# Kernel optimization log

Measured on AMD Instinct MI355X. Metric: run time of the kernel, lower is better.

The kernel has to match this reference:

```python
import jax, jax.numpy as jnp
import numpy as np
import math

IN_FEATURES = 4096
OUT_FEATURES = 4096
TOKENS = 8192


def hadamard(x):
    """Orthonormal fast Walsh-Hadamard transform along last dim (power of two)."""
    n = x.shape[-1]
    orig_shape = x.shape
    y = x.reshape(-1, n)
    h = 1
    while h < n:  # log2(n) butterfly steps (static loop, n known at trace time)
        y = y.reshape(-1, n // (2 * h), 2 * h)
        left = y[..., :h]
        right = y[..., h:2 * h]
        y = jnp.concatenate([left + right, left - right], axis=-1)
        y = y.reshape(-1, n)
        h *= 2
    return (y / math.sqrt(n)).reshape(orig_shape)


def setup_inputs() -> dict:
    key = jax.random.key(0)
    k1, k2, k3, k4 = jax.random.split(key, 4)
    x = jax.random.normal(k1, (TOKENS, IN_FEATURES), dtype=jnp.float32)
    # int8-valued quantized weights, stored as int32 for portability
    Q_tilde = jax.random.randint(k2, (OUT_FEATURES, IN_FEATURES), -127, 128, dtype=jnp.int32)
    # per-row scales, positive, realistic magnitude (~max_abs/127)
    s_tilde = jax.random.uniform(k3, (OUT_FEATURES, 1), dtype=jnp.float32, minval=0.001, maxval=0.02)
    bias = jax.random.normal(k4, (OUT_FEATURES,), dtype=jnp.float32)
    return {"x": x, "Q_tilde": Q_tilde, "s_tilde": s_tilde, "bias": bias}


def reference(x, Q_tilde, s_tilde, bias):
    # y = hadamard(x) @ (Q * s)^T + bias
    xh = hadamard(x)                                      # [T, in]
    W = Q_tilde.astype(jnp.float32) * s_tilde             # [out, in] dequantized
    y = xh @ W.T + bias                                   # [T, out]
    return y
```

## Files before the change

kernel.cpp:

```cpp
#include <hip/hip_runtime.h>
#include <hip/hip_bf16.h>

typedef int   i32x4 __attribute__((ext_vector_type(4)));
typedef unsigned int   u32;
typedef unsigned short u16;
typedef signed char    i8;

#define TOKENS 8192
#define NDIM   4096
#define KDIM   4096
#define BK     64
#define NKT    (KDIM / BK)

__device__ __forceinline__ u32 pack4(int4 q) {
  return (u32)(q.x & 0xff) | ((u32)(q.y & 0xff) << 8) |
         ((u32)(q.z & 0xff) << 16) | ((u32)(q.w & 0xff) << 24);
}

__global__ __launch_bounds__(256)
void fused_aux(const float* __restrict__ x, i8* __restrict__ xq,
               float* __restrict__ xscale,
               const int* __restrict__ Q, i8* __restrict__ W8) {
  __shared__ float tbuf[4 * 65 * 64];

  if (blockIdx.x >= 2048) {
    const size_t idx = (((size_t)(blockIdx.x - 2048)) * 256 + threadIdx.x) * 16;
    int4 a = *reinterpret_cast<const int4*>(Q + idx);
    int4 b = *reinterpret_cast<const int4*>(Q + idx + 4);
    int4 c = *reinterpret_cast<const int4*>(Q + idx + 8);
    int4 d = *reinterpret_cast<const int4*>(Q + idx + 12);
    uint4 pk; pk.x = pack4(a); pk.y = pack4(b); pk.z = pack4(c); pk.w = pack4(d);
    *reinterpret_cast<uint4*>(W8 + idx) = pk;
    return;
  }

  const int wv  = threadIdx.x >> 6;
  const int l   = threadIdx.x & 63;
  const int row = blockIdx.x * 4 + wv;
  float* lb = tbuf + wv * (65 * 64);

  const float4* xv = reinterpret_cast<const float4*>(x + (size_t)row * KDIM) + l * 16;
  float v[64];
#pragma unroll
  for (int j = 0; j < 16; ++j) {
    float4 f = xv[j];
    v[4*j+0] = f.x; v[4*j+1] = f.y; v[4*j+2] = f.z; v[4*j+3] = f.w;
  }

#pragma unroll
  for (int h = 1; h < 64; h <<= 1) {
#pragma unroll
    for (int j = 0; j < 64; ++j) {
      if ((j & h) == 0) {
        float a = v[j], b = v[j + h];
        v[j] = a + b; v[j + h] = a - b;
      }
    }
  }

#pragma unroll
  for (int j = 0; j < 64; ++j)
    lb[l * 65 + j] = v[j];
  asm volatile("s_waitcnt lgkmcnt(0)" ::: "memory");
  __builtin_amdgcn_sched_barrier(0);
  float w[64];
#pragma unroll
  for (int j = 0; j < 64; ++j)
    w[j] = lb[j * 65 + l];

#pragma unroll
  for (int h = 1; h < 64; h <<= 1) {
#pragma unroll
    for (int j = 0; j < 64; ++j) {
      if ((j & h) == 0) {
        float a = w[j], b = w[j + h];
        w[j] = a + b; w[j + h] = a - b;
      }
    }
  }

  float mxu = 0.f;
#pragma unroll
  for (int j = 0; j < 64; ++j) mxu = fmaxf(mxu, fabsf(w[j]));
#pragma unroll
  for (int m = 1; m < 64; m <<= 1) mxu = fmaxf(mxu, __shfl_xor(mxu, m, 64));
  mxu = fmaxf(mxu, 1e-30f);
  const float inv = 127.0f / mxu;

  i8* orow = xq + (size_t)row * KDIM + l;
#pragma unroll
  for (int j = 0; j < 64; ++j) {
    int b = __float2int_rn(w[j] * inv);
    b = min(127, max(-127, b));
    orow[j * 64] = (i8)b;
  }
  if (l == 0) xscale[row] = mxu * (0.015625f / 127.0f);
}

__global__ __launch_bounds__(512, 2)
void gemm256_i8(const i8* __restrict__ A, const i8* __restrict__ B,
                const float* __restrict__ xscale, const float* __restrict__ s,
                const float* __restrict__ bias, float* __restrict__ C) {
  __shared__ __align__(16) i8 lds[4 * 32768];

  const int th   = threadIdx.x;
  const int wave = th >> 6;
  const int lane = th & 63;

  const int b0 = blockIdx.x;
  const int xc = b0 & 7;
  const int i  = b0 >> 3;
  const int mt = i >> 1;
  const int nt = xc * 2 + (i & 1);

  const int srow = th >> 2;
  const int scol = ((th & 3) * 16) ^ (((th >> 5) & 1) << 5);
  const i8* gA0 = A + (size_t)(mt * 256 + srow) * KDIM + scol;
  const i8* gA1 = gA0 + (size_t)128 * KDIM;
  const i8* gB0 = B + (size_t)(nt * 256 + srow) * KDIM + scol;
  const i8* gB1 = gB0 + (size_t)128 * KDIM;

  const int ldsA0 = wave * 1024;
  const int ldsA1 = 8192 + wave * 1024;
  const int ldsB0 = 16384 + wave * 1024;
  const int ldsB1 = 24576 + wave * 1024;

#define STAGE_A(tt, ss) do {                                                    \
    __builtin_amdgcn_global_load_lds(                                           \
      (const __attribute__((address_space(1))) void*)(gA0 + (size_t)(tt) * BK), \
      (__attribute__((address_space(3))) void*)(lds + (ss) * 32768 + ldsA0), 16, 0, 0); \
    __builtin_amdgcn_global_load_lds(                                           \
      (const __attribute__((address_space(1))) void*)(gA1 + (size_t)(tt) * BK), \
      (__attribute__((address_space(3))) void*)(lds + (ss) * 32768 + ldsA1), 16, 0, 0); \
  } while (0)
#define STAGE_B(tt, ss) do {                                                    \
    __builtin_amdgcn_global_load_lds(                                           \
      (const __attribute__((address_space(1))) void*)(gB0 + (size_t)(tt) * BK), \
      (__attribute__((address_space(3))) void*)(lds + (ss) * 32768 + ldsB0), 16, 0, 0); \
    __builtin_amdgcn_global_load_lds(                                           \
      (const __attribute__((address_space(1))) void*)(gB1 + (size_t)(tt) * BK), \
      (__attribute__((address_space(3))) void*)(lds + (ss) * 32768 + ldsB1), 16, 0, 0); \
  } while (0)

  const int wm = wave >> 2;
  const int wn = wave & 3;
  const int laneRow = lane & 15;
  const int kByte   = (lane >> 4) << 4;
  const int swz     = ((lane >> 3) & 1) << 5;
  const int aOff = (((wm * 128 + laneRow) * 64 + kByte) ^ swz);
  const int bOff = (((wn * 64 + laneRow) * 64 + kByte) ^ swz) + 16384;

  i32x4 acc[8][4];
#pragma unroll
  for (int mi = 0; mi < 8; ++mi)
#pragma unroll
    for (int ni = 0; ni < 4; ++ni)
      acc[mi][ni] = i32x4{0, 0, 0, 0};

  STAGE_A(0, 0); STAGE_B(0, 0);
  STAGE_A(1, 1); STAGE_B(1, 1);
  asm volatile("s_waitcnt vmcnt(4)" ::: "memory");
  __builtin_amdgcn_sched_barrier(0);
  __builtin_amdgcn_s_barrier();

  i32x4 afA[4], afB[4], bf0[4], bf1[4];
  {
    const char* c0 = (const char*)lds;
#pragma unroll
    for (int ni = 0; ni < 4; ++ni)
      bf0[ni] = *(const i32x4*)(c0 + bOff + ni * 1024);
#pragma unroll
    for (int mi = 0; mi < 4; ++mi)
      afA[mi] = *(const i32x4*)(c0 + aOff + mi * 1024);
  }

#define TILE(t, BFC, BFN) do {                                                  \
    const char* cur = (const char*)lds + ((t) & 3) * 32768;                     \
    const char* nxt = (const char*)lds + (((t) + 1) & 3) * 32768;               \
    _Pragma("unroll")                                                           \
    for (int mi = 0; mi < 4; ++mi)                                              \
      afB[mi] = *(const i32x4*)(cur + aOff + 4096 + mi * 1024);                 \
    if ((t) + 2 < NKT) STAGE_A((t) + 2, ((t) + 2) & 3);                         \
    asm volatile("s_waitcnt lgkmcnt(4)" ::: "memory");                          \
    __builtin_amdgcn_sched_barrier(0);                                          \
    __builtin_amdgcn_s_setprio(1);                                              \
    _Pragma("unroll")                                                           \
    for (int mi = 0; mi < 4; ++mi)                                              \
      _Pragma("unroll")                                                         \
      for (int ni = 0; ni < 4; ++ni)                                            \
        acc[mi][ni] = __builtin_amdgcn_mfma_i32_16x16x64_i8(afA[mi], BFC[ni],   \
                                                            acc[mi][ni], 0, 0, 0); \
    __builtin_amdgcn_s_setprio(0);                                              \
    if ((t) + 1 < NKT) {                                                        \
      if ((t) + 2 < NKT) { asm volatile("s_waitcnt vmcnt(2)" ::: "memory"); }   \
      else               { asm volatile("s_waitcnt vmcnt(0)" ::: "memory"); }   \
      __builtin_amdgcn_sched_barrier(0);                                        \
      __builtin_amdgcn_s_barrier();                                             \
      _Pragma("unroll")                                                         \
      for (int ni = 0; ni < 4; ++ni)                                            \
        BFN[ni] = *(const i32x4*)(nxt + bOff + ni * 1024);                      \
      _Pragma("unroll")                                                         \
      for (int mi = 0; mi < 4; ++mi)                                            \
        afA[mi] = *(const i32x4*)(nxt + aOff + mi * 1024);                      \
      if ((t) + 2 < NKT) STAGE_B((t) + 2, ((t) + 2) & 3);                       \
      asm volatile("s_waitcnt lgkmcnt(8)" ::: "memory");                        \
      __builtin_amdgcn_sched_barrier(0);                                        \
    } else {                                                                    \
      asm volatile("s_waitcnt lgkmcnt(0)" ::: "memory");                        \
      __builtin_amdgcn_sched_barrier(0);                                        \
    }                                                                           \
    __builtin_amdgcn_s_setprio(1);                                              \
    _Pragma("unroll")                                                           \
    for (int mi = 0; mi < 4; ++mi)                                              \
      _Pragma("unroll")                                                         \
      for (int ni = 0; ni < 4; ++ni)                                            \
        acc[mi + 4][ni] = __builtin_amdgcn_mfma_i32_16x16x64_i8(afB[mi], BFC[ni], \
                                                            acc[mi + 4][ni], 0, 0, 0); \
    __builtin_amdgcn_s_setprio(0);                                              \
  } while (0)

  for (int t = 0; t < NKT; t += 2) {
    TILE(t,     bf0, bf1);
    TILE(t + 1, bf1, bf0);
  }
#undef TILE
#undef STAGE_A
#undef STAGE_B

  const int col0 = nt * 256 + wn * 64 + (lane & 15);
  const int row0 = mt * 256 + wm * 128 + ((lane >> 4) << 2);
  float xs[4][8];
#pragma unroll
  for (int mi = 0; mi < 8; ++mi)
#pragma unroll
    for (int r = 0; r < 4; ++r)
      xs[r][mi] = xscale[row0 + mi * 16 + r];
#pragma unroll
  for (int ni = 0; ni < 4; ++ni) {
    const float sc = s[col0 + ni * 16];
    const float bv = bias[col0 + ni * 16];
#pragma unroll
    for (int mi = 0; mi < 8; ++mi) {
      float* cp = C + (size_t)(row0 + mi * 16) * NDIM + col0 + ni * 16;
#pragma unroll
      for (int r = 0; r < 4; ++r)
        cp[(size_t)r * NDIM] = (float)acc[mi][ni][r] * (xs[r][mi] * sc) + bv;
    }
  }
}

extern "C" void kernel_launch(void* const* d_in, const int* in_sizes, int n_in,
                              void* d_out, int out_size, void* d_ws, size_t ws_size,
                              hipStream_t stream) {
  (void)in_sizes; (void)n_in; (void)out_size; (void)ws_size;
  const float* x    = (const float*)d_in[0];
  const int*   Q    = (const int*)d_in[1];
  const float* s    = (const float*)d_in[2];
  const float* bias = (const float*)d_in[3];
  float* out = (float*)d_out;

  i8*    xq     = (i8*)d_ws;
  i8*    W8     = xq + (size_t)TOKENS * KDIM;
  float* xscale = (float*)(W8 + (size_t)NDIM * KDIM);

  fused_aux<<<dim3(6144), dim3(256), 0, stream>>>(x, xq, xscale, Q, W8);
  gemm256_i8<<<dim3((TOKENS / 256) * (NDIM / 256)), dim3(512), 0, stream>>>(
      xq, W8, xscale, s, bias, out);
}
```

Before: 193.7 us.

## Switch int8 GEMM to 32x32x32 MFMA with new LDS swizzle and K-split pipeline

Replaces the 16x16x64 int8 MFMA tiles with 32x32x32 int8 MFMA instructions, splitting each 64-wide K tile into two 32-byte halves loaded from LDS in an alternating software pipeline. The LDS swizzle pattern and the staging column XOR are changed to match the new fragment access pattern, and the epilogue is rewritten for the 32x32 accumulator layout. The aim is fewer MFMA issues and fewer LDS fragment loads per FLOP. The trade-off is longer-latency instructions and an epilogue that re-reads xscale per element instead of caching it in registers.

```diff
diff --git a/kernel.cpp b/kernel.cpp
--- a/kernel.cpp
+++ b/kernel.cpp
@@ -1,7 +1,8 @@
 #include <hip/hip_runtime.h>
 #include <hip/hip_bf16.h>
 
-typedef int   i32x4 __attribute__((ext_vector_type(4)));
+typedef int   i32x4  __attribute__((ext_vector_type(4)));
+typedef int   i32x16 __attribute__((ext_vector_type(16)));
 typedef unsigned int   u32;
 typedef unsigned short u16;
 typedef signed char    i8;
@@ -98,9 +99,9 @@
 }
 
 __global__ __launch_bounds__(512, 2)
-void gemm256_i8(const i8* __restrict__ A, const i8* __restrict__ B,
-                const float* __restrict__ xscale, const float* __restrict__ s,
-                const float* __restrict__ bias, float* __restrict__ C) {
+void gemm32_i8(const i8* __restrict__ A, const i8* __restrict__ B,
+               const float* __restrict__ xscale, const float* __restrict__ s,
+               const float* __restrict__ bias, float* __restrict__ C) {
   __shared__ __align__(16) i8 lds[4 * 32768];
 
   const int th   = threadIdx.x;
@@ -114,7 +115,7 @@
   const int nt = xc * 2 + (i & 1);
 
   const int srow = th >> 2;
-  const int scol = ((th & 3) * 16) ^ (((th >> 5) & 1) << 5);
+  const int scol = ((th & 3) * 16) ^ (((th >> 3) & 3) << 4);
   const i8* gA0 = A + (size_t)(mt * 256 + srow) * KDIM + scol;
   const i8* gA1 = gA0 + (size_t)128 * KDIM;
   const i8* gB0 = B + (size_t)(nt * 256 + srow) * KDIM + scol;
@@ -142,20 +143,24 @@
       (__attribute__((address_space(3))) void*)(lds + (ss) * 32768 + ldsB1), 16, 0, 0); \
   } while (0)
 
-  const int wm = wave >> 2;
-  const int wn = wave & 3;
-  const int laneRow = lane & 15;
-  const int kByte   = (lane >> 4) << 4;
-  const int swz     = ((lane >> 3) & 1) << 5;
-  const int aOff = (((wm * 128 + laneRow) * 64 + kByte) ^ swz);
-  const int bOff = (((wn * 64 + laneRow) * 64 + kByte) ^ swz) + 16384;
-
-  i32x4 acc[8][4];
-#pragma unroll
-  for (int mi = 0; mi < 8; ++mi)
-#pragma unroll
-    for (int ni = 0; ni < 4; ++ni)
-      acc[mi][ni] = i32x4{0, 0, 0, 0};
+  const int wm  = wave >> 2;
+  const int wn  = wave & 3;
+  const int l31 = lane & 31;
+  const int lh  = lane >> 5;
+  const int swz = ((l31 >> 1) & 3) << 4;
+  const int colK0 = (lh * 16) ^ swz;
+  const int colK1 = (32 + lh * 16) ^ swz;
+  const int aBase = (wm * 128 + l31) * 64;
+  const int bBase = (wn * 64  + l31) * 64 + 16384;
+
+  i32x16 acc[4][2];
+#pragma unroll
+  for (int mb = 0; mb < 4; ++mb)
+#pragma unroll
+    for (int nb = 0; nb < 2; ++nb)
+#pragma unroll
+      for (int r = 0; r < 16; ++r)
+        acc[mb][nb][r] = 0;
 
   STAGE_A(0, 0); STAGE_B(0, 0);
   STAGE_A(1, 1); STAGE_B(1, 1);
@@ -163,88 +168,86 @@
   __builtin_amdgcn_sched_barrier(0);
   __builtin_amdgcn_s_barrier();
 
-  i32x4 afA[4], afB[4], bf0[4], bf1[4];
+  i32x4 aK0[4], bK0[2], aK1[4], bK1[2];
   {
     const char* c0 = (const char*)lds;
 #pragma unroll
-    for (int ni = 0; ni < 4; ++ni)
-      bf0[ni] = *(const i32x4*)(c0 + bOff + ni * 1024);
-#pragma unroll
-    for (int mi = 0; mi < 4; ++mi)
-      afA[mi] = *(const i32x4*)(c0 + aOff + mi * 1024);
-  }
-
-#define TILE(t, BFC, BFN) do {                                                  \
-    const char* cur = (const char*)lds + ((t) & 3) * 32768;                     \
-    const char* nxt = (const char*)lds + (((t) + 1) & 3) * 32768;               \
-    _Pragma("unroll")                                                           \
-    for (int mi = 0; mi < 4; ++mi)                                              \
-      afB[mi] = *(const i32x4*)(cur + aOff + 4096 + mi * 1024);                 \
-    if ((t) + 2 < NKT) STAGE_A((t) + 2, ((t) + 2) & 3);                         \
-    asm volatile("s_waitcnt lgkmcnt(4)" ::: "memory");                          \
-    __builtin_amdgcn_sched_barrier(0);                                          \
-    __builtin_amdgcn_s_setprio(1);                                              \
-    _Pragma("unroll")                                                           \
-    for (int mi = 0; mi < 4; ++mi)                                              \
-      _Pragma("unroll")                                                         \
-      for (int ni = 0; ni < 4; ++ni)                                            \
-        acc[mi][ni] = __builtin_amdgcn_mfma_i32_16x16x64_i8(afA[mi], BFC[ni],   \
-                                                            acc[mi][ni], 0, 0, 0); \
-    __builtin_amdgcn_s_setprio(0);                                              \
-    if ((t) + 1 < NKT) {                                                        \
-      if ((t) + 2 < NKT) { asm volatile("s_waitcnt vmcnt(2)" ::: "memory"); }   \
-      else               { asm volatile("s_waitcnt vmcnt(0)" ::: "memory"); }   \
-      __builtin_amdgcn_sched_barrier(0);                                        \
-      __builtin_amdgcn_s_barrier();                                             \
-      _Pragma("unroll")                                                         \
-      for (int ni = 0; ni < 4; ++ni)                                            \
-        BFN[ni] = *(const i32x4*)(nxt + bOff + ni * 1024);                      \
-      _Pragma("unroll")                                                         \
-      for (int mi = 0; mi < 4; ++mi)                                            \
-        afA[mi] = *(const i32x4*)(nxt + aOff + mi * 1024);                      \
-      if ((t) + 2 < NKT) STAGE_B((t) + 2, ((t) + 2) & 3);                       \
-      asm volatile("s_waitcnt lgkmcnt(8)" ::: "memory");                        \
-      __builtin_amdgcn_sched_barrier(0);                                        \
-    } else {                                                                    \
-      asm volatile("s_waitcnt lgkmcnt(0)" ::: "memory");                        \
-      __builtin_amdgcn_sched_barrier(0);                                        \
-    }                                                                           \
-    __builtin_amdgcn_s_setprio(1);                                              \
-    _Pragma("unroll")                                                           \
-    for (int mi = 0; mi < 4; ++mi)                                              \
-      _Pragma("unroll")                                                         \
-      for (int ni = 0; ni < 4; ++ni)                                            \
-        acc[mi + 4][ni] = __builtin_amdgcn_mfma_i32_16x16x64_i8(afB[mi], BFC[ni], \
-                                                            acc[mi + 4][ni], 0, 0, 0); \
-    __builtin_amdgcn_s_setprio(0);                                              \
-  } while (0)
-
-  for (int t = 0; t < NKT; t += 2) {
-    TILE(t,     bf0, bf1);
-    TILE(t + 1, bf1, bf0);
-  }
-#undef TILE
+    for (int nb = 0; nb < 2; ++nb)
+      bK0[nb] = *(const i32x4*)(c0 + bBase + nb * 2048 + colK0);
+#pragma unroll
+    for (int mb = 0; mb < 4; ++mb)
+      aK0[mb] = *(const i32x4*)(c0 + aBase + mb * 2048 + colK0);
+  }
+
+  for (int t = 0; t < NKT; ++t) {
+    const char* cur = (const char*)lds + (t & 3) * 32768;
+    const char* nxt = (const char*)lds + ((t + 1) & 3) * 32768;
+
+#pragma unroll
+    for (int nb = 0; nb < 2; ++nb)
+      bK1[nb] = *(const i32x4*)(cur + bBase + nb * 2048 + colK1);
+#pragma unroll
+    for (int mb = 0; mb < 4; ++mb)
+      aK1[mb] = *(const i32x4*)(cur + aBase + mb * 2048 + colK1);
+    if (t + 2 < NKT) STAGE_A(t + 2, (t + 2) & 3);
+    asm volatile("s_waitcnt lgkmcnt(6)" ::: "memory");
+    __builtin_amdgcn_sched_barrier(0);
+    __builtin_amdgcn_s_setprio(1);
+#pragma unroll
+    for (int mb = 0; mb < 4; ++mb)
+#pragma unroll
+      for (int nb = 0; nb < 2; ++nb)
+        acc[mb][nb] = __builtin_amdgcn_mfma_i32_32x32x32_i8(aK0[mb], bK0[nb], acc[mb][nb], 0, 0, 0);
+    __builtin_amdgcn_s_setprio(0);
+
+    if (t + 2 < NKT)      { asm volatile("s_waitcnt vmcnt(2)" ::: "memory"); }
+    else if (t + 1 < NKT) { asm volatile("s_waitcnt vmcnt(0)" ::: "memory"); }
+    __builtin_amdgcn_sched_barrier(0);
+    if (t + 1 < NKT) {
+      __builtin_amdgcn_s_barrier();
+#pragma unroll
+      for (int nb = 0; nb < 2; ++nb)
+        bK0[nb] = *(const i32x4*)(nxt + bBase + nb * 2048 + colK0);
+#pragma unroll
+      for (int mb = 0; mb < 4; ++mb)
+        aK0[mb] = *(const i32x4*)(nxt + aBase + mb * 2048 + colK0);
+      if (t + 2 < NKT) STAGE_B(t + 2, (t + 2) & 3);
+      asm volatile("s_waitcnt lgkmcnt(6)" ::: "memory");
+      __builtin_amdgcn_sched_barrier(0);
+    } else {
+      asm volatile("s_waitcnt lgkmcnt(0)" ::: "memory");
+      __builtin_amdgcn_sched_barrier(0);
+    }
+    __builtin_amdgcn_s_setprio(1);
+#pragma unroll
+    for (int mb = 0; mb < 4; ++mb)
+#pragma unroll
+      for (int nb = 0; nb < 2; ++nb)
+        acc[mb][nb] = __builtin_amdgcn_mfma_i32_32x32x32_i8(aK1[mb], bK1[nb], acc[mb][nb], 0, 0, 0);
+    __builtin_amdgcn_s_setprio(0);
+  }
 #undef STAGE_A
 #undef STAGE_B
 
-  const int col0 = nt * 256 + wn * 64 + (lane & 15);
-  const int row0 = mt * 256 + wm * 128 + ((lane >> 4) << 2);
-  float xs[4][8];
-#pragma unroll
-  for (int mi = 0; mi < 8; ++mi)
-#pragma unroll
-    for (int r = 0; r < 4; ++r)
-      xs[r][mi] = xscale[row0 + mi * 16 + r];
-#pragma unroll
-  for (int ni = 0; ni < 4; ++ni) {
-    const float sc = s[col0 + ni * 16];
-    const float bv = bias[col0 + ni * 16];
-#pragma unroll
-    for (int mi = 0; mi < 8; ++mi) {
-      float* cp = C + (size_t)(row0 + mi * 16) * NDIM + col0 + ni * 16;
-#pragma unroll
-      for (int r = 0; r < 4; ++r)
-        cp[(size_t)r * NDIM] = (float)acc[mi][ni][r] * (xs[r][mi] * sc) + bv;
+  const int col0 = nt * 256 + wn * 64 + l31;
+  const int row0 = mt * 256 + wm * 128 + lh * 4;
+#pragma unroll
+  for (int nb = 0; nb < 2; ++nb) {
+    const int colb = col0 + nb * 32;
+    const float sc = s[colb];
+    const float bv = bias[colb];
+#pragma unroll
+    for (int mb = 0; mb < 4; ++mb) {
+#pragma unroll
+      for (int q = 0; q < 4; ++q) {
+        const int rbase = row0 + mb * 32 + q * 8;
+#pragma unroll
+        for (int r = 0; r < 4; ++r) {
+          const int row = rbase + r;
+          C[(size_t)row * NDIM + colb] =
+              (float)acc[mb][nb][q * 4 + r] * (xscale[row] * sc) + bv;
+        }
+      }
     }
   }
 }
@@ -264,6 +267,6 @@
   float* xscale = (float*)(W8 + (size_t)NDIM * KDIM);
 
   fused_aux<<<dim3(6144), dim3(256), 0, stream>>>(x, xq, xscale, Q, W8);
-  gemm256_i8<<<dim3((TOKENS / 256) * (NDIM / 256)), dim3(512), 0, stream>>>(
+  gemm32_i8<<<dim3((TOKENS / 256) * (NDIM / 256)), dim3(512), 0, stream>>>(
       xq, W8, xscale, s, bias, out);
 }
```

Result: slower. 201.4 us (+4.0%).
